# Optimization experiments

Measured on AMD Instinct MI355X. Metric: run time of the kernel, lower is better.

The kernel has to match this reference:

```python
import jax, jax.numpy as jnp
import numpy as np

B, K, N, E, D = 32, 32, 2048, 16384, 768
L_GNN, L_TR, H = 2, 4, 12
FF, VOCAB, N_ROLES, MAX_POS, N_HOPS = 3072, 25, 2, 64, 16


def setup_inputs() -> dict:
    key = jax.random.key(0)
    ks = jax.random.split(key, 32)
    s = 0.02
    inp = {
        "raw_features": jax.random.normal(ks[0], (B, K, D), jnp.float32),
        "x0": jax.random.randint(ks[1], (K, N), 0, VOCAB),
        "edge0": jax.random.randint(ks[2], (K, 2, E), 0, N),
        "batch0": jnp.sort(jax.random.randint(ks[3], (K, N), 0, B), axis=-1),
        "x1": jax.random.randint(ks[4], (K, N), 0, VOCAB),
        "edge1": jax.random.randint(ks[5], (K, 2, E), 0, N),
        "batch1": jnp.sort(jax.random.randint(ks[6], (K, N), 0, B), axis=-1),
        "role_ids": jax.random.randint(ks[7], (B, K), 0, N_ROLES),
        "position_ids": jax.random.randint(ks[8], (B, K), 0, MAX_POS),
        "hop_ids": jax.random.randint(ks[9], (B, K), 0, N_HOPS),
        # GNNForProtein params (shared across slots and both proteins)
        "amino_embed": jax.random.normal(ks[10], (VOCAB, D)) * s,
        "gnn_W": jax.random.normal(ks[11], (L_GNN, D, D)) * s,
        "gnn_b": jnp.zeros((L_GNN, D)),
        # GraphBert embeddings
        "role_emb": jax.random.normal(ks[12], (N_ROLES, D)) * s,
        "pos_emb": jax.random.normal(ks[13], (MAX_POS, D)) * s,
        "hop_emb": jax.random.normal(ks[14], (N_HOPS, D)) * s,
        "emb_ln_scale": jnp.ones((D,)),
        "emb_ln_bias": jnp.zeros((D,)),
        # GraphBert transformer layers (stacked over L_TR)
        "Wq": jax.random.normal(ks[15], (L_TR, D, D)) * s,
        "bq": jnp.zeros((L_TR, D)),
        "Wk": jax.random.normal(ks[16], (L_TR, D, D)) * s,
        "bk": jnp.zeros((L_TR, D)),
        "Wv": jax.random.normal(ks[17], (L_TR, D, D)) * s,
        "bv": jnp.zeros((L_TR, D)),
        "Wo": jax.random.normal(ks[18], (L_TR, D, D)) * s,
        "bo": jnp.zeros((L_TR, D)),
        "ln1_s": jnp.ones((L_TR, D)),
        "ln1_b": jnp.zeros((L_TR, D)),
        "W1": jax.random.normal(ks[19], (L_TR, D, FF)) * s,
        "b1": jnp.zeros((L_TR, FF)),
        "W2": jax.random.normal(ks[20], (L_TR, FF, D)) * s,
        "b2": jnp.zeros((L_TR, D)),
        "ln2_s": jnp.ones((L_TR, D)),
        "ln2_b": jnp.zeros((L_TR, D)),
    }
    return inp


def _ln(x, s, b):
    m = jnp.mean(x, -1, keepdims=True)
    v = jnp.mean(jnp.square(x - m), -1, keepdims=True)
    return (x - m) * jax.lax.rsqrt(v + 1e-12) * s + b


def _gnn(node_ids, edges, batch_idx, amino_embed, W, b):
    # One protein slot: GCN message passing + mean readout per graph in batch.
    h = amino_embed[node_ids]                      # [N, D]
    src, dst = edges[0], edges[1]
    for l in range(W.shape[0]):
        agg = jax.ops.segment_sum(h[src], dst, num_segments=N)
        h = jax.nn.relu((h + agg) @ W[l] + b[l])
    sums = jax.ops.segment_sum(h, batch_idx, num_segments=B)
    cnt = jax.ops.segment_sum(jnp.ones((h.shape[0], 1), h.dtype), batch_idx, num_segments=B)
    return sums / jnp.maximum(cnt, 1.0)           # [B, D]


def reference(raw_features, x0, edge0, batch0, x1, edge1, batch1, role_ids, position_ids, hop_ids,
              amino_embed, gnn_W, gnn_b, role_emb, pos_emb, hop_emb, emb_ln_scale, emb_ln_bias,
              Wq, bq, Wk, bk, Wv, bv, Wo, bo, ln1_s, ln1_b, W1, b1, W2, b2, ln2_s, ln2_b):
    # vmap over the K protein slots replaces the original Python loop (same math).
    gnn_v = jax.vmap(_gnn, in_axes=(0, 0, 0, None, None, None))
    p0 = gnn_v(x0, edge0, batch0, amino_embed, gnn_W, gnn_b)   # [K, B, D]
    p1 = gnn_v(x1, edge1, batch1, amino_embed, gnn_W, gnn_b)   # [K, B, D]
    feats = raw_features + jnp.transpose(p0 + p1, (1, 0, 2))   # [B, K, D]
    # GraphBert embeddings + encoder
    h = feats + role_emb[role_ids] + pos_emb[position_ids] + hop_emb[hop_ids]
    h = _ln(h, emb_ln_scale, emb_ln_bias)
    dh = D // H
    scale = float(1.0 / np.sqrt(dh))
    for l in range(Wq.shape[0]):
        q = (h @ Wq[l] + bq[l]).reshape(B, K, H, dh)
        kk = (h @ Wk[l] + bk[l]).reshape(B, K, H, dh)
        v = (h @ Wv[l] + bv[l]).reshape(B, K, H, dh)
        att = jax.nn.softmax(jnp.einsum('bqhd,bkhd->bhqk', q, kk) * scale, axis=-1)
        ctx = jnp.einsum('bhqk,bkhd->bqhd', att, v).reshape(B, K, D)
        h = _ln(h + ctx @ Wo[l] + bo[l], ln1_s[l], ln1_b[l])
        f = jax.nn.gelu(h @ W1[l] + b1[l]) @ W2[l] + b2[l]
        h = _ln(h + f, ln2_s[l], ln2_b[l])
    return h
```

## Files before the change

### kernel.cpp

```cpp
#include <hip/hip_runtime.h>
#include <hip/hip_bf16.h>
#include <math.h>

using bf16 = __hip_bfloat16;
typedef __attribute__((ext_vector_type(8))) short short8;
typedef __attribute__((ext_vector_type(4))) float floatx4;
typedef __attribute__((ext_vector_type(4))) short short4v;

#define NB   32
#define NK   32
#define NNODE 2048
#define NEDGE 16384
#define ND   768
#define NHH  12
#define DHH  64
#define NFF  3072
#define NG   64
#define LTR  4
#define VOCAB 25

static __device__ __forceinline__ float b2f(bf16 x) { return __bfloat162float(x); }
static __device__ __forceinline__ bf16 f2b(float x) { return __float2bfloat16(x); }
static __device__ __forceinline__ float bs2f(short s) {
    unsigned u = ((unsigned)(unsigned short)s) << 16;
    float f; __builtin_memcpy(&f, &u, 4); return f;
}
static __device__ __forceinline__ short f2bs(float x) {
    bf16 h = f2b(x); short s; __builtin_memcpy(&s, &h, 2); return s;
}

static __device__ __forceinline__ void load_lds16(const bf16* g, bf16* l) {
    __builtin_amdgcn_global_load_lds((const __attribute__((address_space(1))) void*)g,
                                     (__attribute__((address_space(3))) void*)l, 16, 0, 0);
}

static __device__ __forceinline__ float ldf(const void* p, size_t i, bool f32) {
    return f32 ? ((const float*)p)[i] : b2f(((const bf16*)p)[i]);
}

__global__ void detect_dtype_kernel(const void* __restrict__ eln_s, int* __restrict__ flag) {
    if (threadIdx.x == 0 && blockIdx.x == 0) {
        unsigned w = ((const unsigned*)eln_s)[0];
        flag[0] = (w == 0x3F800000u) ? 1 : 0;
    }
}

__device__ __forceinline__ void conv_tile(const void* __restrict__ src, size_t srcOff,
                                          bf16* __restrict__ dst, int R, int Cn,
                                          int tr, int tc, bool f32, int t,
                                          short (*tile)[70]) {
    int r0 = tr * 64, c0 = tc * 64;
    int rr = t >> 4, c4 = (t & 15) * 4;
    #pragma unroll
    for (int p = 0; p < 4; ++p) {
        int r = rr + p * 16;
        size_t base = srcOff + (size_t)(r0 + r) * Cn + c0 + c4;
        short4v s;
        if (f32) {
            float4 v = *(const float4*)((const float*)src + base);
            s.x = f2bs(v.x); s.y = f2bs(v.y); s.z = f2bs(v.z); s.w = f2bs(v.w);
        } else {
            s = *(const short4v*)((const short*)src + base);
        }
        tile[r][c4]     = s.x; tile[r][c4 + 1] = s.y;
        tile[r][c4 + 2] = s.z; tile[r][c4 + 3] = s.w;
    }
    __syncthreads();
    #pragma unroll
    for (int p = 0; p < 4; ++p) {
        int c = rr + p * 16;
        short4v o;
        o.x = tile[c4][c];     o.y = tile[c4 + 1][c];
        o.z = tile[c4 + 2][c]; o.w = tile[c4 + 3][c];
        *(short4v*)((short*)dst + (size_t)(c0 + c) * R + r0 + c4) = o;
    }
}

__global__ __launch_bounds__(256) void convert_gnn_kernel(const void* __restrict__ gnnW,
                                                          bf16* __restrict__ gnnT,
                                                          const int* __restrict__ flag) {
    __shared__ short tile[64][70];
    bool f32 = flag[0] != 0;
    int bid = blockIdx.x;
    int id = bid / 144, tl = bid % 144;
    conv_tile(gnnW, (size_t)id * 589824, gnnT + (size_t)id * 589824,
              768, 768, tl / 12, tl % 12, f32, threadIdx.x, tile);
}

__global__ __launch_bounds__(256) void convert_layer_kernel(
    const void* __restrict__ Wq, const void* __restrict__ Wk, const void* __restrict__ Wv,
    const void* __restrict__ Wo, const void* __restrict__ W1, const void* __restrict__ W2,
    int l, bf16* __restrict__ qkvT, bf16* __restrict__ oT,
    bf16* __restrict__ w1T, bf16* __restrict__ w2T, const int* __restrict__ flag) {
    __shared__ short tile[64][70];
    bool f32 = flag[0] != 0;
    int bid = blockIdx.x, t = threadIdx.x;
    if (bid < 432) {
        int m = bid / 144, tl = bid % 144;
        const void* src = (m == 0) ? Wq : ((m == 1) ? Wk : Wv);
        conv_tile(src, (size_t)l * 589824, qkvT + (size_t)m * 589824,
                  768, 768, tl / 12, tl % 12, f32, t, tile);
    } else if (bid < 576) {
        int tl = bid - 432;
        conv_tile(Wo, (size_t)l * 589824, oT, 768, 768, tl / 12, tl % 12, f32, t, tile);
    } else if (bid < 1152) {
        int tl = bid - 576;
        conv_tile(W1, (size_t)l * 768 * 3072, w1T, 768, 3072, tl / 48, tl % 48, f32, t, tile);
    } else {
        int tl = bid - 1152;
        conv_tile(W2, (size_t)l * 3072 * 768, w2T, 3072, 768, tl / 12, tl % 12, f32, t, tile);
    }
}

__global__ __launch_bounds__(256) void pack_bias_kernel(
    const void* __restrict__ gnnb, const void* __restrict__ bq, const void* __restrict__ bk,
    const void* __restrict__ bv, const void* __restrict__ bo, const void* __restrict__ b1,
    const void* __restrict__ b2, float* __restrict__ out, const int* __restrict__ flag) {
    bool f32 = flag[0] != 0;
    int i = blockIdx.x * 256 + threadIdx.x;
    if (i >= 1536 + LTR * 6912) return;
    float v;
    if (i < 1536) v = ldf(gnnb, i, f32);
    else {
        int j = i - 1536, l = j / 6912, r = j % 6912;
        if      (r <  768) v = ldf(bq, l * 768 + r, f32);
        else if (r < 1536) v = ldf(bk, l * 768 + r - 768, f32);
        else if (r < 2304) v = ldf(bv, l * 768 + r - 1536, f32);
        else if (r < 3072) v = ldf(bo, l * 768 + r - 2304, f32);
        else if (r < 6144) v = ldf(b1, l * 3072 + r - 3072, f32);
        else               v = ldf(b2, l * 768 + r - 6144, f32);
    }
    out[i] = v;
}

__global__ __launch_bounds__(192) void e1_kernel(const void* __restrict__ emb,
                                                 const bf16* __restrict__ w0T,
                                                 bf16* __restrict__ E1,
                                                 const int* __restrict__ flag) {
    bool f32 = flag[0] != 0;
    int v = blockIdx.x, t = threadIdx.x;
    float acc[4] = {0.f, 0.f, 0.f, 0.f};
    for (int k = 0; k < ND; k += 4) {
        float e0 = ldf(emb, (size_t)v * ND + k,     f32);
        float e1 = ldf(emb, (size_t)v * ND + k + 1, f32);
        float e2 = ldf(emb, (size_t)v * ND + k + 2, f32);
        float e3 = ldf(emb, (size_t)v * ND + k + 3, f32);
        #pragma unroll
        for (int j = 0; j < 4; ++j) {
            const short4v w = *(const short4v*)&w0T[(size_t)(t * 4 + j) * ND + k];
            acc[j] += e0 * bs2f(w.x) + e1 * bs2f(w.y) + e2 * bs2f(w.z) + e3 * bs2f(w.w);
        }
    }
    short4v o; o.x = f2bs(acc[0]); o.y = f2bs(acc[1]); o.z = f2bs(acc[2]); o.w = f2bs(acc[3]);
    ((short4v*)(E1 + (size_t)v * ND))[t] = o;
}

__global__ __launch_bounds__(256) void count_deg_kernel(const int* __restrict__ edge0,
                                                        const int* __restrict__ edge1,
                                                        int* __restrict__ deg) {
    int gid = blockIdx.x;
    int g = gid >> 6, chunk = gid & 63;
    const int* ep = (g < NK) ? (edge0 + (size_t)g * 2 * NEDGE)
                             : (edge1 + (size_t)(g - NK) * 2 * NEDGE);
    int e = chunk * 256 + threadIdx.x;
    int dst = ep[NEDGE + e];
    atomicAdd(&deg[g * NNODE + dst], 1);
}

__global__ __launch_bounds__(256) void scan_deg_kernel(int* __restrict__ deg,
                                                       int* __restrict__ indptr) {
    int g = blockIdx.x, t = threadIdx.x;
    __shared__ int sums[256];
    int loc[8]; int s = 0;
    #pragma unroll
    for (int i = 0; i < 8; ++i) { loc[i] = deg[g * NNODE + t * 8 + i]; s += loc[i]; }
    sums[t] = s; __syncthreads();
    for (int off = 1; off < 256; off <<= 1) {
        int v = (t >= off) ? sums[t - off] : 0;
        __syncthreads();
        sums[t] += v;
        __syncthreads();
    }
    int run = sums[t] - s;
    #pragma unroll
    for (int i = 0; i < 8; ++i) {
        indptr[g * (NNODE + 1) + t * 8 + i] = run;
        deg[g * NNODE + t * 8 + i] = run;
        run += loc[i];
    }
    if (t == 255) indptr[g * (NNODE + 1) + NNODE] = run;
}

__global__ __launch_bounds__(256) void fill_csr_kernel(const int* __restrict__ edge0,
                                                       const int* __restrict__ edge1,
                                                       int* __restrict__ cursor,
                                                       int* __restrict__ csr_src) {
    int gid = blockIdx.x;
    int g = gid >> 6, chunk = gid & 63;
    const int* ep = (g < NK) ? (edge0 + (size_t)g * 2 * NEDGE)
                             : (edge1 + (size_t)(g - NK) * 2 * NEDGE);
    int e = chunk * 256 + threadIdx.x;
    int src = ep[e];
    int dst = ep[NEDGE + e];
    int p = atomicAdd(&cursor[g * NNODE + dst], 1);
    csr_src[(size_t)g * NEDGE + p] = src;
}

__global__ __launch_bounds__(64) void batch_count_kernel(const int* __restrict__ batch0,
                                                         const int* __restrict__ batch1,
                                                         int* __restrict__ cnt) {
    int g = blockIdx.x;
    int b = threadIdx.x;
    if (b >= NB) return;
    const int* bp = (g < NK) ? (batch0 + (size_t)g * NNODE)
                             : (batch1 + (size_t)(g - NK) * NNODE);
    int lo = 0, hi = NNODE;
    while (lo < hi) { int mid = (lo + hi) >> 1; if (bp[mid] < b) lo = mid + 1; else hi = mid; }
    int start = lo;
    hi = NNODE;
    while (lo < hi) { int mid = (lo + hi) >> 1; if (bp[mid] < b + 1) lo = mid + 1; else hi = mid; }
    cnt[g * NB + b] = lo - start;
}

static __device__ __forceinline__ void node_block_decode(int id, int& gl, int& n) {
    int r = id & 7, q = id >> 3;
    gl = r + 8 * (q >> 11);
    n = q & 2047;
}

__global__ __launch_bounds__(192) void gnn_layer1_kernel(const int* __restrict__ x0,
                                                         const int* __restrict__ x1,
                                                         const bf16* __restrict__ E1,
                                                         const float* __restrict__ b0,
                                                         const int* __restrict__ indptr,
                                                         const int* __restrict__ csr_src,
                                                         bf16* __restrict__ hC, int g0) {
    int gl, n; node_block_decode(blockIdx.x, gl, n);
    int g = g0 + gl;
    const int* xg = (g < NK) ? (x0 + (size_t)g * NNODE) : (x1 + (size_t)(g - NK) * NNODE);
    int beg = indptr[g * (NNODE + 1) + n];
    int end = indptr[g * (NNODE + 1) + n + 1];
    const int* cs = csr_src + (size_t)g * NEDGE;
    int t = threadIdx.x;
    const short4v* E = (const short4v*)E1;
    short4v v = E[(size_t)xg[n] * 192 + t];
    float a0 = bs2f(v.x), a1 = bs2f(v.y), a2 = bs2f(v.z), a3 = bs2f(v.w);
    for (int e = beg; e < end; ++e) {
        int s = cs[e];
        short4v w = E[(size_t)xg[s] * 192 + t];
        a0 += bs2f(w.x); a1 += bs2f(w.y); a2 += bs2f(w.z); a3 += bs2f(w.w);
    }
    float4 bb = ((const float4*)b0)[t];
    short4v o;
    o.x = f2bs(fmaxf(a0 + bb.x, 0.f));
    o.y = f2bs(fmaxf(a1 + bb.y, 0.f));
    o.z = f2bs(fmaxf(a2 + bb.z, 0.f));
    o.w = f2bs(fmaxf(a3 + bb.w, 0.f));
    ((short4v*)(hC + ((size_t)gl * NNODE + n) * ND))[t] = o;
}

__global__ __launch_bounds__(192) void gnn_aggregate_kernel(const bf16* __restrict__ hC,
                                                            const int* __restrict__ indptr,
                                                            const int* __restrict__ csr_src,
                                                            bf16* __restrict__ xC, int g0) {
    int gl, n; node_block_decode(blockIdx.x, gl, n);
    int g = g0 + gl;
    int beg = indptr[g * (NNODE + 1) + n];
    int end = indptr[g * (NNODE + 1) + n + 1];
    const short4v* hg = (const short4v*)(hC + (size_t)gl * NNODE * ND);
    const int* cs = csr_src + (size_t)g * NEDGE;
    int t = threadIdx.x;
    short4v v = hg[(size_t)n * 192 + t];
    float a0 = bs2f(v.x), a1 = bs2f(v.y), a2 = bs2f(v.z), a3 = bs2f(v.w);
    for (int e = beg; e < end; ++e) {
        int s = cs[e];
        short4v w = hg[(size_t)s * 192 + t];
        a0 += bs2f(w.x); a1 += bs2f(w.y); a2 += bs2f(w.z); a3 += bs2f(w.w);
    }
    short4v o; o.x = f2bs(a0); o.y = f2bs(a1); o.z = f2bs(a2); o.w = f2bs(a3);
    ((short4v*)(xC + ((size_t)gl * NNODE + n) * ND))[t] = o;
}

__global__ __launch_bounds__(512) void gemm8_pool(const bf16* __restrict__ A,
                                                  const bf16* __restrict__ BT,
                                                  const float* __restrict__ bias,
                                                  int M, int K, int N,
                                                  const int* __restrict__ batAp,
                                                  const int* __restrict__ batBp,
                                                  float* __restrict__ pool, int g0) {
    __shared__ bf16 sA[3][256][64];
    __shared__ bf16 sB[2][128][64];
    const int nt = K >> 6;
    int nTN = N >> 7;
    int xcd = blockIdx.x & 7, jb = blockIdx.x >> 3;
    int brow = (jb / nTN) * 8 + xcd;
    int bcol = jb % nTN;
    const int row0 = brow << 8, col0 = bcol << 7;
    int t = threadIdx.x;
    int wid = t >> 6, lane = t & 63;
    int wr = wid >> 1, wc = wid & 1;
    int l15 = lane & 15, kx = lane >> 4, sw = lane & 7;

    const bf16* Abase = A + (size_t)row0 * K;
    const bf16* Bbase = BT + (size_t)col0 * K;

    auto stage = [&](const bf16* g, bf16* slot, int r0) {
        int r = r0 + (t >> 3);
        int ks = ((t & 7) ^ ((t >> 3) & 7)) << 3;
        load_lds16(g + (size_t)r * K + ks, slot + ((size_t)r0 << 6) + ((size_t)t << 3));
    };
    auto rdA = [&](int s, int i, int kh) {
        return *(const short8*)&sA[s][wr * 64 + i * 16 + l15][(((kh << 2) | kx) ^ sw) << 3];
    };
    auto rdB = [&](int s, int j, int kh) {
        return *(const short8*)&sB[s][wc * 64 + j * 16 + l15][(((kh << 2) | kx) ^ sw) << 3];
    };

    stage(Abase, &sA[0][0][0], 0);   stage(Abase, &sA[0][0][0], 64);
    stage(Abase, &sA[0][0][0], 128); stage(Abase, &sA[0][0][0], 192);
    stage(Bbase, &sB[0][0][0], 0);   stage(Bbase, &sB[0][0][0], 64);
    const bf16* gA1 = Abase + 64;
    stage(gA1, &sA[1][0][0], 0);   stage(gA1, &sA[1][0][0], 64);
    stage(gA1, &sA[1][0][0], 128); stage(gA1, &sA[1][0][0], 192);
    asm volatile("s_waitcnt vmcnt(4)" ::: "memory");
    __builtin_amdgcn_s_barrier();

    floatx4 acc[4][4] = {};
    for (int kt = 0; kt < nt; ++kt) {
        int sa = kt % 3, sb = kt & 1;
        bf16* saN = &sA[(kt + 2) % 3][0][0];
        const bf16* gA = Abase + (kt + 2) * 64;
        short8 af[4], bf[4];
        #pragma unroll
        for (int i = 0; i < 4; ++i) af[i] = rdA(sa, i, 0);
        #pragma unroll
        for (int j = 0; j < 4; ++j) bf[j] = rdB(sb, j, 0);
        if (kt + 1 < nt) {
            const bf16* gB = Bbase + (kt + 1) * 64;
            bf16* sbN = &sB[(kt + 1) & 1][0][0];
            stage(gB, sbN, 0); stage(gB, sbN, 64);
        }
        if (kt + 2 < nt) { stage(gA, saN, 0); stage(gA, saN, 64); }
        __builtin_amdgcn_s_barrier();
        asm volatile("s_waitcnt lgkmcnt(0)" ::: "memory");
        __builtin_amdgcn_s_setprio(1);
        #pragma unroll
        for (int i = 0; i < 4; ++i)
            #pragma unroll
            for (int j = 0; j < 4; ++j)
                acc[i][j] = __builtin_amdgcn_mfma_f32_16x16x32_bf16(af[i], bf[j], acc[i][j], 0, 0, 0);
        __builtin_amdgcn_s_setprio(0);
        __builtin_amdgcn_s_barrier();
        #pragma unroll
        for (int i = 0; i < 4; ++i) af[i] = rdA(sa, i, 1);
        #pragma unroll
        for (int j = 0; j < 4; ++j) bf[j] = rdB(sb, j, 1);
        if (kt + 2 < nt) { stage(gA, saN, 128); stage(gA, saN, 192); }
        __builtin_amdgcn_s_barrier();
        asm volatile("s_waitcnt lgkmcnt(0)" ::: "memory");
        __builtin_amdgcn_s_setprio(1);
        #pragma unroll
        for (int i = 0; i < 4; ++i)
            #pragma unroll
            for (int j = 0; j < 4; ++j)
                acc[i][j] = __builtin_amdgcn_mfma_f32_16x16x32_bf16(af[i], bf[j], acc[i][j], 0, 0, 0);
        __builtin_amdgcn_s_setprio(0);
        if (kt + 1 < nt) {
            if (kt + 2 < nt) asm volatile("s_waitcnt vmcnt(4)" ::: "memory");
            else             asm volatile("s_waitcnt vmcnt(0)" ::: "memory");
            __builtin_amdgcn_s_barrier();
        }
    }

    __syncthreads();
    int g = g0 + (row0 >> 11);
    const int* bp = (g < NK) ? (batAp + (size_t)g * NNODE)
                             : (batBp + (size_t)(g - NK) * NNODE);
    int nbase = row0 & (NNODE - 1);
    float* pg = pool + (size_t)g * NB * ND;
    int cb = wc * 64 + l15;
    float bv[4];
    #pragma unroll
    for (int j = 0; j < 4; ++j) bv[j] = bias[col0 + cb + j * 16];
    float* lp = (float*)sA;
    int bLo = bp[nbase], bHi = bp[nbase + 255];
    int nb = (bHi - bLo + 1) * 128;
    for (int idx = t; idx < nb; idx += 512) lp[idx] = 0.f;
    __syncthreads();
    float sums[4] = {0.f, 0.f, 0.f, 0.f};
    int curb = -1;
    #pragma unroll
    for (int i = 0; i < 4; ++i) {
        int rr = nbase + wr * 64 + i * 16 + kx * 4;
        #pragma unroll
        for (int r = 0; r < 4; ++r) {
            int b = bp[rr + r];
            if (b != curb) {
                if (curb >= 0) {
                    #pragma unroll
                    for (int j = 0; j < 4; ++j)
                        atomicAdd(&lp[(curb - bLo) * 128 + cb + j * 16], sums[j]);
                }
                curb = b;
                sums[0] = sums[1] = sums[2] = sums[3] = 0.f;
            }
            #pragma unroll
            for (int j = 0; j < 4; ++j)
                sums[j] += fmaxf(acc[i][j][r] + bv[j], 0.f);
        }
    }
    #pragma unroll
    for (int j = 0; j < 4; ++j)
        atomicAdd(&lp[(curb - bLo) * 128 + cb + j * 16], sums[j]);
    __syncthreads();
    for (int idx = t; idx < nb; idx += 512) {
        float v = lp[idx];
        if (v != 0.f)
            atomicAdd(&pg[(size_t)(bLo + (idx >> 7)) * ND + col0 + (idx & 127)], v);
    }
}

__global__ __launch_bounds__(256) void gemm_tn_sk(const bf16* __restrict__ A,
                                                  const bf16* __restrict__ BT,
                                                  const float* __restrict__ bias,
                                                  void* __restrict__ C,
                                                  int M, int K, int N, int splitK,
                                                  int act, int store) {
    __shared__ bf16 lA[2][64][32];
    __shared__ bf16 lB[2][128][32];
    int nTilesN = N >> 7, nTilesM = M >> 6;
    int tiles = nTilesM * nTilesN;
    int split = blockIdx.x / tiles;
    int jt = blockIdx.x % tiles;
    int brow = jt / nTilesN, bcol = jt % nTilesN;
    int t = threadIdx.x;
    int wave = t >> 6, lane = t & 63;
    int wr = wave >> 1, wc = wave & 1;
    int l15 = lane & 15, quad = lane >> 4;
    const int row0 = brow << 6, col0 = bcol << 7;
    const int kLen = K / splitK, kBeg = split * kLen;
    const int sr0 = t >> 2, sk0 = (t & 3) * 8;
    const bf16* Ab = A + (size_t)(row0 + sr0) * K + kBeg + sk0;
    const bf16* Bb = BT + (size_t)(col0 + sr0) * K + kBeg + sk0;
    const size_t rstride = (size_t)64 * K;

    load_lds16(Ab,           &lA[0][sr0][sk0]);
    load_lds16(Bb,           &lB[0][sr0][sk0]);
    load_lds16(Bb + rstride, &lB[0][sr0 + 64][sk0]);

    floatx4 acc[2][4] = {};
    int cur = 0;
    for (int k0 = 0; k0 < kLen; k0 += 32) {
        __syncthreads();
        if (k0 + 32 < kLen) {
            load_lds16(Ab + k0 + 32,           &lA[cur ^ 1][sr0][sk0]);
            load_lds16(Bb + k0 + 32,           &lB[cur ^ 1][sr0][sk0]);
            load_lds16(Bb + rstride + k0 + 32, &lB[cur ^ 1][sr0 + 64][sk0]);
        }
        short8 afr[2], bfr[4];
        #pragma unroll
        for (int i = 0; i < 2; ++i)
            afr[i] = *reinterpret_cast<const short8*>(&lA[cur][wr * 32 + i * 16 + l15][quad * 8]);
        #pragma unroll
        for (int j = 0; j < 4; ++j)
            bfr[j] = *reinterpret_cast<const short8*>(&lB[cur][wc * 64 + j * 16 + l15][quad * 8]);
        #pragma unroll
        for (int i = 0; i < 2; ++i)
            #pragma unroll
            for (int j = 0; j < 4; ++j)
                acc[i][j] = __builtin_amdgcn_mfma_f32_16x16x32_bf16(afr[i], bfr[j], acc[i][j], 0, 0, 0);
        cur ^= 1;
    }
    #pragma unroll
    for (int i = 0; i < 2; ++i) {
        int rbase = row0 + wr * 32 + i * 16 + quad * 4;
        #pragma unroll
        for (int j = 0; j < 4; ++j) {
            int c = col0 + wc * 64 + j * 16 + l15;
            float bv = (split == 0) ? bias[c] : 0.f;
            #pragma unroll
            for (int r = 0; r < 4; ++r) {
                float v = acc[i][j][r] + bv;
                if (act == 1) v = fmaxf(v, 0.f);
                else if (act == 2) {
                    float x = v;
                    float u = 1.5957691216057308f * (x + 0.044715f * x * x * x);
                    v = x / (1.f + __expf(-u));
                }
                size_t idx = (size_t)(rbase + r) * N + c;
                if (store == 0)      atomicAdd(&((float*)C)[idx], v);
                else if (store == 1) ((float*)C)[idx] = v;
                else                 ((bf16*)C)[idx] = f2b(v);
            }
        }
    }
}

__device__ __forceinline__ void block_ln_768(float (&x)[3], int t,
                                             const void* __restrict__ s,
                                             const void* __restrict__ b,
                                             size_t sOff, bool f32,
                                             float (&y)[3], float* red) {
    float loc = x[0] + x[1] + x[2];
    red[t] = loc; __syncthreads();
    for (int off = 128; off > 0; off >>= 1) {
        if (t < off) red[t] += red[t + off];
        __syncthreads();
    }
    float mean = red[0] * (1.f / 768.f);
    __syncthreads();
    float vs = 0.f;
    #pragma unroll
    for (int e = 0; e < 3; ++e) { float d = x[e] - mean; vs += d * d; }
    red[t] = vs; __syncthreads();
    for (int off = 128; off > 0; off >>= 1) {
        if (t < off) red[t] += red[t + off];
        __syncthreads();
    }
    float var = red[0] * (1.f / 768.f);
    __syncthreads();
    float inv = rsqrtf(var + 1e-12f);
    #pragma unroll
    for (int e = 0; e < 3; ++e) {
        int d = t + e * 256;
        y[e] = (x[e] - mean) * inv * ldf(s, sOff + d, f32) + ldf(b, sOff + d, f32);
    }
}

__global__ __launch_bounds__(256) void combine_embed_ln_kernel(
    const void* __restrict__ raw, const float* __restrict__ pooled,
    const int* __restrict__ cnt,
    const int* __restrict__ role_ids, const int* __restrict__ pos_ids, const int* __restrict__ hop_ids,
    const void* __restrict__ role_emb, const void* __restrict__ pos_emb, const void* __restrict__ hop_emb,
    const void* __restrict__ lns, const void* __restrict__ lnb,
    float* __restrict__ hT, bf16* __restrict__ hbf,
    const int* __restrict__ flag) {
    bool f32 = flag[0] != 0;
    __shared__ float red[256];
    int token = blockIdx.x;
    int b = token >> 5, k = token & 31;
    int t = threadIdx.x;
    int rid = role_ids[b * NK + k];
    int pid = pos_ids[b * NK + k];
    int hid = hop_ids[b * NK + k];
    float inv0 = 1.f / (float)max(cnt[k * NB + b], 1);
    float inv1 = 1.f / (float)max(cnt[(NK + k) * NB + b], 1);
    float x[3], y[3];
    #pragma unroll
    for (int e = 0; e < 3; ++e) {
        int d = t + e * 256;
        float p0 = pooled[((size_t)k * NB + b) * ND + d] * inv0;
        float p1 = pooled[((size_t)(NK + k) * NB + b) * ND + d] * inv1;
        x[e] = ldf(raw, (size_t)token * ND + d, f32) + p0 + p1
             + ldf(role_emb, (size_t)rid * ND + d, f32)
             + ldf(pos_emb, (size_t)pid * ND + d, f32)
             + ldf(hop_emb, (size_t)hid * ND + d, f32);
    }
    block_ln_768(x, t, lns, lnb, 0, f32, y, red);
    #pragma unroll
    for (int e = 0; e < 3; ++e) {
        int d = t + e * 256;
        hT[(size_t)token * ND + d] = y[e];
        hbf[(size_t)token * ND + d] = f2b(y[e]);
    }
}

__global__ __launch_bounds__(256) void add_ln_kernel(float* __restrict__ hT,
                                                     const void* __restrict__ lns,
                                                     const void* __restrict__ lnb,
                                                     unsigned long long sOff,
                                                     void* __restrict__ outp, int extOut,
                                                     const int* __restrict__ flag) {
    bool f32 = flag[0] != 0;
    __shared__ float red[256];
    int token = blockIdx.x;
    int t = threadIdx.x;
    float x[3], y[3];
    #pragma unroll
    for (int e = 0; e < 3; ++e) {
        int d = t + e * 256;
        x[e] = hT[(size_t)token * ND + d];
    }
    block_ln_768(x, t, lns, lnb, sOff, f32, y, red);
    #pragma unroll
    for (int e = 0; e < 3; ++e) {
        int d = t + e * 256;
        size_t idx = (size_t)token * ND + d;
        hT[idx] = y[e];
        if (extOut && f32) ((float*)outp)[idx] = y[e];
        else               ((bf16*)outp)[idx] = f2b(y[e]);
    }
}

__global__ __launch_bounds__(256) void attn_kernel(const bf16* __restrict__ qkv,
                                                   bf16* __restrict__ ctx) {
    int blk = blockIdx.x;
    int b = blk / NHH, h = blk % NHH;
    __shared__ float lq[NK][DHH], lk[NK][DHH], lv[NK][DHH];
    __shared__ float ls[NK][NK];
    int t = threadIdx.x;
    {
        int tok = t >> 3, d8 = (t & 7) * 8;
        size_t base = ((size_t)(b * NK + tok)) * (3 * ND) + h * DHH + d8;
        short8 q8 = *(const short8*)&qkv[base];
        short8 k8 = *(const short8*)&qkv[base + ND];
        short8 v8 = *(const short8*)&qkv[base + 2 * ND];
        #pragma unroll
        for (int j = 0; j < 8; ++j) {
            lq[tok][d8 + j] = bs2f(q8[j]);
            lk[tok][d8 + j] = bs2f(k8[j]);
            lv[tok][d8 + j] = bs2f(v8[j]);
        }
    }
    __syncthreads();
    const float scale = 0.125f;
    for (int i = t; i < NK * NK; i += 256) {
        int qi = i >> 5, kj = i & 31;
        float s = 0.f;
        #pragma unroll
        for (int d = 0; d < DHH; ++d) s += lq[qi][d] * lk[kj][d];
        ls[qi][kj] = s * scale;
    }
    __syncthreads();
    if (t < NK) {
        float m = -1e30f;
        for (int j = 0; j < NK; ++j) m = fmaxf(m, ls[t][j]);
        float sum = 0.f;
        for (int j = 0; j < NK; ++j) { float e = expf(ls[t][j] - m); ls[t][j] = e; sum += e; }
        float inv = 1.f / sum;
        for (int j = 0; j < NK; ++j) ls[t][j] *= inv;
    }
    __syncthreads();
    for (int i = t; i < NK * DHH; i += 256) {
        int qi = i >> 6, d = i & 63;
        float s = 0.f;
        #pragma unroll
        for (int j = 0; j < NK; ++j) s += ls[qi][j] * lv[j][d];
        ctx[((size_t)(b * NK + qi)) * ND + h * DHH + d] = f2b(s);
    }
}

extern "C" void kernel_launch(void* const* d_in, const int* in_sizes, int n_in,
                              void* d_out, int out_size, void* d_ws, size_t ws_size,
                              hipStream_t stream) {
    const void* raw      = d_in[0];
    const int*  x0       = (const int*)d_in[1];
    const int*  edge0    = (const int*)d_in[2];
    const int*  batch0   = (const int*)d_in[3];
    const int*  x1       = (const int*)d_in[4];
    const int*  edge1    = (const int*)d_in[5];
    const int*  batch1   = (const int*)d_in[6];
    const int*  role_ids = (const int*)d_in[7];
    const int*  pos_ids  = (const int*)d_in[8];
    const int*  hop_ids  = (const int*)d_in[9];
    const void* amino    = d_in[10];
    const void* gnnW     = d_in[11];
    const void* gnnb     = d_in[12];
    const void* role_emb = d_in[13];
    const void* pos_emb  = d_in[14];
    const void* hop_emb  = d_in[15];
    const void* eln_s    = d_in[16];
    const void* eln_b    = d_in[17];
    const void* Wq       = d_in[18];
    const void* bq       = d_in[19];
    const void* Wk       = d_in[20];
    const void* bk       = d_in[21];
    const void* Wv       = d_in[22];
    const void* bv       = d_in[23];
    const void* Wo       = d_in[24];
    const void* bo       = d_in[25];
    const void* ln1_s    = d_in[26];
    const void* ln1_b    = d_in[27];
    const void* W1       = d_in[28];
    const void* b1       = d_in[29];
    const void* W2       = d_in[30];
    const void* b2       = d_in[31];
    const void* ln2_s    = d_in[32];
    const void* ln2_b    = d_in[33];

    char* ws = (char*)d_ws;
    size_t off = 0;
    auto alloc = [&](size_t bytes) -> void* {
        void* p = ws + off;
        off = (off + bytes + 255) & ~(size_t)255;
        return p;
    };
    int*   dflag   = (int*)alloc(256);
    float* pooled  = (float*)alloc((size_t)NG * NB * ND * 4);
    int*   cntb    = (int*)alloc((size_t)NG * NB * 4);
    int*   indptr  = (int*)alloc((size_t)NG * (NNODE + 1) * 4);
    int*   csr_src = (int*)alloc((size_t)NG * NEDGE * 4);
    int*   degcur  = (int*)alloc((size_t)NG * NNODE * 4);
    bf16*  gnnT    = (bf16*)alloc((size_t)2 * ND * ND * 2);
    bf16*  E1      = (bf16*)alloc((size_t)VOCAB * ND * 2);
    float* biasPk  = (float*)alloc((size_t)(1536 + LTR * 6912) * 4);
    const size_t QS = (size_t)3 * ND * ND, OS = (size_t)ND * ND;
    const size_t S1 = (size_t)ND * NFF,    S2 = (size_t)NFF * ND;
    bf16*  qkvT    = (bf16*)alloc(QS * 2);
    bf16*  oT      = (bf16*)alloc(OS * 2);
    bf16*  w1T     = (bf16*)alloc(S1 * 2);
    bf16*  w2T     = (bf16*)alloc(S2 * 2);

    const size_t perG  = (size_t)NNODE * ND * 2;
    const size_t bigTR = 21 * 1024 * 1024;
    int gc = 8;
    for (int cand = 32; cand >= 8; cand >>= 1) {
        size_t bigGNN = 2 * (size_t)cand * perG;
        size_t need = off + (bigGNN > bigTR ? bigGNN : bigTR) + (1 << 20);
        if (need <= ws_size) { gc = cand; break; }
    }
    char* bigbase = (char*)alloc(2 * (size_t)gc * perG > bigTR ? 2 * (size_t)gc * perG : bigTR);
    bf16* hC = (bf16*)bigbase;
    bf16* xC = (bf16*)(bigbase + (size_t)gc * perG);
    size_t toff = 0;
    auto talloc = [&](size_t bytes) -> void* {
        void* p = bigbase + toff;
        toff = (toff + bytes + 255) & ~(size_t)255;
        return p;
    };
    float* hT    = (float*)talloc((size_t)NB * NK * ND * 4);
    bf16*  hbf   = (bf16*)talloc((size_t)NB * NK * ND * 2);
    bf16*  qkvb  = (bf16*)talloc((size_t)NB * NK * 3 * ND * 2);
    bf16*  ctxb  = (bf16*)talloc((size_t)NB * NK * ND * 2);
    bf16*  ffbuf = (bf16*)talloc((size_t)NB * NK * NFF * 2);

    auto gemm_sk = [&](const bf16* A, const bf16* BT, const float* bias, void* C,
                       int Mm, int Kk, int Nn, int splitK, int act, int store) {
        int blocks = (Mm >> 6) * (Nn >> 7) * splitK;
        gemm_tn_sk<<<blocks, 256, 0, stream>>>(A, BT, bias, C, Mm, Kk, Nn, splitK, act, store);
    };

    detect_dtype_kernel<<<1, 64, 0, stream>>>(eln_s, dflag);

    convert_gnn_kernel<<<288, 256, 0, stream>>>(gnnW, gnnT, dflag);
    pack_bias_kernel<<<(1536 + LTR * 6912 + 255) / 256, 256, 0, stream>>>(
        gnnb, bq, bk, bv, bo, b1, b2, biasPk, dflag);
    e1_kernel<<<VOCAB, 192, 0, stream>>>(amino, gnnT, E1, dflag);

    hipMemsetAsync(degcur, 0, (size_t)NG * NNODE * 4, stream);
    hipMemsetAsync(pooled, 0, (size_t)NG * NB * ND * 4, stream);
    count_deg_kernel<<<NG * 64, 256, 0, stream>>>(edge0, edge1, degcur);
    scan_deg_kernel<<<NG, 256, 0, stream>>>(degcur, indptr);
    fill_csr_kernel<<<NG * 64, 256, 0, stream>>>(edge0, edge1, degcur, csr_src);
    batch_count_kernel<<<NG, 64, 0, stream>>>(batch0, batch1, cntb);

    for (int g0 = 0; g0 < NG; g0 += gc) {
        gnn_layer1_kernel<<<gc * NNODE, 192, 0, stream>>>(x0, x1, E1, biasPk,
                                                          indptr, csr_src, hC, g0);
        gnn_aggregate_kernel<<<gc * NNODE, 192, 0, stream>>>(hC, indptr, csr_src, xC, g0);
        int blocks = ((gc * NNODE) >> 8) * (ND >> 7);
        gemm8_pool<<<blocks, 512, 0, stream>>>(xC, gnnT + (size_t)ND * ND, biasPk + ND,
                                               gc * NNODE, ND, ND,
                                               batch0, batch1, pooled, g0);
    }

    combine_embed_ln_kernel<<<NB * NK, 256, 0, stream>>>(
        raw, pooled, cntb, role_ids, pos_ids, hop_ids,
        role_emb, pos_emb, hop_emb, eln_s, eln_b, hT, hbf, dflag);

    const int M = NB * NK;
    for (int l = 0; l < LTR; ++l) {
        convert_layer_kernel<<<1728, 256, 0, stream>>>(Wq, Wk, Wv, Wo, W1, W2, l,
                                                       qkvT, oT, w1T, w2T, dflag);
        const float* lb = biasPk + 1536 + l * 6912;
        gemm_sk(hbf, qkvT, lb, qkvb, M, ND, 3 * ND, 1, 0, 2);
        attn_kernel<<<NB * NHH, 256, 0, stream>>>(qkvb, ctxb);
        gemm_sk(ctxb, oT, lb + 2304, hT, M, ND, ND, 2, 0, 0);
        add_ln_kernel<<<M, 256, 0, stream>>>(hT, ln1_s, ln1_b,
                                             (unsigned long long)l * ND, hbf, 0, dflag);
        gemm_sk(hbf, w1T, lb + 3072, ffbuf, M, ND, NFF, 1, 2, 2);
        gemm_sk(ffbuf, w2T, lb + 6144, hT, M, NFF, ND, 4, 0, 0);
        int ext = (l == LTR - 1) ? 1 : 0;
        void* outb = ext ? d_out : (void*)hbf;
        add_ln_kernel<<<M, 256, 0, stream>>>(hT, ln2_s, ln2_b,
                                             (unsigned long long)l * ND, outb, ext, dflag);
    }
}
```

Before: 1.373 ms.

## Widen GNN gather loads to 16 bytes and deepen transformer GEMM K-tile with swizzle

The GNN layer-1 and aggregate kernels now handle two nodes per 192-thread block. Each thread loads 8 bf16 values at once, and the edge loop is unrolled by two so more gathers are in flight. The split-K transformer GEMM moves from a 32-wide to a 64-wide K tile, with XOR-swizzled LDS staging to avoid bank conflicts and one barrier per tile instead of per 32-K step. This trades higher LDS usage and more registers for fewer synchronisations and wider memory transactions.

```diff
diff --git a/kernel.cpp b/kernel.cpp
--- a/kernel.cpp
+++ b/kernel.cpp
@@ -222,12 +222,6 @@
     cnt[g * NB + b] = lo - start;
 }
 
-static __device__ __forceinline__ void node_block_decode(int id, int& gl, int& n) {
-    int r = id & 7, q = id >> 3;
-    gl = r + 8 * (q >> 11);
-    n = q & 2047;
-}
-
 __global__ __launch_bounds__(192) void gnn_layer1_kernel(const int* __restrict__ x0,
                                                          const int* __restrict__ x1,
                                                          const bf16* __restrict__ E1,
@@ -235,50 +229,83 @@
                                                          const int* __restrict__ indptr,
                                                          const int* __restrict__ csr_src,
                                                          bf16* __restrict__ hC, int g0) {
-    int gl, n; node_block_decode(blockIdx.x, gl, n);
+    int id = blockIdx.x;
+    int r = id & 7, q = id >> 3;
+    int gl = r + 8 * (q >> 10);
+    int np = q & 1023;
+    int t = threadIdx.x;
+    int j = t / 96, ln = t % 96;
+    int n = np * 2 + j;
     int g = g0 + gl;
     const int* xg = (g < NK) ? (x0 + (size_t)g * NNODE) : (x1 + (size_t)(g - NK) * NNODE);
     int beg = indptr[g * (NNODE + 1) + n];
     int end = indptr[g * (NNODE + 1) + n + 1];
     const int* cs = csr_src + (size_t)g * NEDGE;
-    int t = threadIdx.x;
-    const short4v* E = (const short4v*)E1;
-    short4v v = E[(size_t)xg[n] * 192 + t];
-    float a0 = bs2f(v.x), a1 = bs2f(v.y), a2 = bs2f(v.z), a3 = bs2f(v.w);
-    for (int e = beg; e < end; ++e) {
-        int s = cs[e];
-        short4v w = E[(size_t)xg[s] * 192 + t];
-        a0 += bs2f(w.x); a1 += bs2f(w.y); a2 += bs2f(w.z); a3 += bs2f(w.w);
-    }
-    float4 bb = ((const float4*)b0)[t];
-    short4v o;
-    o.x = f2bs(fmaxf(a0 + bb.x, 0.f));
-    o.y = f2bs(fmaxf(a1 + bb.y, 0.f));
-    o.z = f2bs(fmaxf(a2 + bb.z, 0.f));
-    o.w = f2bs(fmaxf(a3 + bb.w, 0.f));
-    ((short4v*)(hC + ((size_t)gl * NNODE + n) * ND))[t] = o;
+    const short8* E = (const short8*)E1;
+    short8 v = E[(size_t)xg[n] * 96 + ln];
+    float a[8];
+    #pragma unroll
+    for (int u = 0; u < 8; ++u) a[u] = bs2f(v[u]);
+    int e = beg;
+    for (; e + 1 < end; e += 2) {
+        int s1 = cs[e], s2 = cs[e + 1];
+        short8 w1 = E[(size_t)xg[s1] * 96 + ln];
+        short8 w2 = E[(size_t)xg[s2] * 96 + ln];
+        #pragma unroll
+        for (int u = 0; u < 8; ++u) a[u] += bs2f(w1[u]) + bs2f(w2[u]);
+    }
+    if (e < end) {
+        short8 w = E[(size_t)xg[cs[e]] * 96 + ln];
+        #pragma unroll
+        for (int u = 0; u < 8; ++u) a[u] += bs2f(w[u]);
+    }
+    float4 ba = ((const float4*)b0)[ln * 2];
+    float4 bb = ((const float4*)b0)[ln * 2 + 1];
+    short8 o;
+    o[0] = f2bs(fmaxf(a[0] + ba.x, 0.f)); o[1] = f2bs(fmaxf(a[1] + ba.y, 0.f));
+    o[2] = f2bs(fmaxf(a[2] + ba.z, 0.f)); o[3] = f2bs(fmaxf(a[3] + ba.w, 0.f));
+    o[4] = f2bs(fmaxf(a[4] + bb.x, 0.f)); o[5] = f2bs(fmaxf(a[5] + bb.y, 0.f));
+    o[6] = f2bs(fmaxf(a[6] + bb.z, 0.f)); o[7] = f2bs(fmaxf(a[7] + bb.w, 0.f));
+    ((short8*)(hC + ((size_t)gl * NNODE + n) * ND))[ln] = o;
 }
 
 __global__ __launch_bounds__(192) void gnn_aggregate_kernel(const bf16* __restrict__ hC,
                                                             const int* __restrict__ indptr,
                                                             const int* __restrict__ csr_src,
                                                             bf16* __restrict__ xC, int g0) {
-    int gl, n; node_block_decode(blockIdx.x, gl, n);
+    int id = blockIdx.x;
+    int r = id & 7, q = id >> 3;
+    int gl = r + 8 * (q >> 10);
+    int np = q & 1023;
+    int t = threadIdx.x;
+    int j = t / 96, ln = t % 96;
+    int n = np * 2 + j;
     int g = g0 + gl;
     int beg = indptr[g * (NNODE + 1) + n];
     int end = indptr[g * (NNODE + 1) + n + 1];
-    const short4v* hg = (const short4v*)(hC + (size_t)gl * NNODE * ND);
+    const short8* hg = (const short8*)(hC + (size_t)gl * NNODE * ND);
     const int* cs = csr_src + (size_t)g * NEDGE;
-    int t = threadIdx.x;
-    short4v v = hg[(size_t)n * 192 + t];
-    float a0 = bs2f(v.x), a1 = bs2f(v.y), a2 = bs2f(v.z), a3 = bs2f(v.w);
-    for (int e = beg; e < end; ++e) {
-        int s = cs[e];
-        short4v w = hg[(size_t)s * 192 + t];
-        a0 += bs2f(w.x); a1 += bs2f(w.y); a2 += bs2f(w.z); a3 += bs2f(w.w);
-    }
-    short4v o; o.x = f2bs(a0); o.y = f2bs(a1); o.z = f2bs(a2); o.w = f2bs(a3);
-    ((short4v*)(xC + ((size_t)gl * NNODE + n) * ND))[t] = o;
+    short8 v = hg[(size_t)n * 96 + ln];
+    float a[8];
+    #pragma unroll
+    for (int u = 0; u < 8; ++u) a[u] = bs2f(v[u]);
+    int e = beg;
+    for (; e + 1 < end; e += 2) {
+        int s1 = cs[e], s2 = cs[e + 1];
+        short8 w1 = hg[(size_t)s1 * 96 + ln];
+        short8 w2 = hg[(size_t)s2 * 96 + ln];
+        #pragma unroll
+        for (int u = 0; u < 8; ++u) a[u] += bs2f(w1[u]) + bs2f(w2[u]);
+    }
+    if (e < end) {
+        short8 w = hg[(size_t)cs[e] * 96 + ln];
+        #pragma unroll
+        for (int u = 0; u < 8; ++u) a[u] += bs2f(w[u]);
+    }
+    short8 o;
+    #pragma unroll
+    for (int u = 0; u < 8; ++u) o[u] = f2bs(a[u]);
+    ((short8*)(xC + ((size_t)gl * NNODE + n) * ND))[ln] = o;
 }
 
 __global__ __launch_bounds__(512) void gemm8_pool(const bf16* __restrict__ A,
@@ -426,54 +453,68 @@
                                                   void* __restrict__ C,
                                                   int M, int K, int N, int splitK,
                                                   int act, int store) {
-    __shared__ bf16 lA[2][64][32];
-    __shared__ bf16 lB[2][128][32];
-    int nTilesN = N >> 7, nTilesM = M >> 6;
-    int tiles = nTilesM * nTilesN;
+    __shared__ bf16 lA[2][64][64];
+    __shared__ bf16 lB[2][128][64];
+    int nTN = N >> 7, nTM = M >> 6;
+    int tiles = nTM * nTN;
     int split = blockIdx.x / tiles;
     int jt = blockIdx.x % tiles;
-    int brow = jt / nTilesN, bcol = jt % nTilesN;
+    int brow = jt / nTN, bcol = jt % nTN;
     int t = threadIdx.x;
     int wave = t >> 6, lane = t & 63;
     int wr = wave >> 1, wc = wave & 1;
-    int l15 = lane & 15, quad = lane >> 4;
+    int l15 = lane & 15, kx = lane >> 4, sw = lane & 7;
     const int row0 = brow << 6, col0 = bcol << 7;
     const int kLen = K / splitK, kBeg = split * kLen;
-    const int sr0 = t >> 2, sk0 = (t & 3) * 8;
-    const bf16* Ab = A + (size_t)(row0 + sr0) * K + kBeg + sk0;
-    const bf16* Bb = BT + (size_t)(col0 + sr0) * K + kBeg + sk0;
-    const size_t rstride = (size_t)64 * K;
-
-    load_lds16(Ab,           &lA[0][sr0][sk0]);
-    load_lds16(Bb,           &lB[0][sr0][sk0]);
-    load_lds16(Bb + rstride, &lB[0][sr0 + 64][sk0]);
+    const int nt = kLen >> 6;
+    const bf16* Abase = A + (size_t)row0 * K + kBeg;
+    const bf16* Bbase = BT + (size_t)col0 * K + kBeg;
+
+    auto stage = [&](const bf16* gsrc, bf16* slot, int r0) {
+        int rr = r0 + (t >> 3);
+        int ks = ((t & 7) ^ (rr & 7)) << 3;
+        load_lds16(gsrc + (size_t)rr * K + ks, slot + ((size_t)r0 << 6) + ((size_t)t << 3));
+    };
+    auto stageTile = [&](int kt, int buf) {
+        const bf16* gA = Abase + kt * 64;
+        const bf16* gB = Bbase + kt * 64;
+        stage(gA, &lA[buf][0][0], 0);  stage(gA, &lA[buf][0][0], 32);
+        stage(gB, &lB[buf][0][0], 0);  stage(gB, &lB[buf][0][0], 32);
+        stage(gB, &lB[buf][0][0], 64); stage(gB, &lB[buf][0][0], 96);
+    };
+    auto rdA = [&](int s, int i, int kh) {
+        return *(const short8*)&lA[s][wr * 32 + i * 16 + l15][(((kh << 2) | kx) ^ sw) << 3];
+    };
+    auto rdB = [&](int s, int jj, int kh) {
+        return *(const short8*)&lB[s][wc * 64 + jj * 16 + l15][(((kh << 2) | kx) ^ sw) << 3];
+    };
+
+    stageTile(0, 0);
+    __syncthreads();
 
     floatx4 acc[2][4] = {};
     int cur = 0;
-    for (int k0 = 0; k0 < kLen; k0 += 32) {
+    for (int kt = 0; kt < nt; ++kt) {
+        if (kt + 1 < nt) stageTile(kt + 1, cur ^ 1);
+        #pragma unroll
+        for (int kh = 0; kh < 2; ++kh) {
+            short8 af[2], bf2[4];
+            #pragma unroll
+            for (int i = 0; i < 2; ++i) af[i] = rdA(cur, i, kh);
+            #pragma unroll
+            for (int jj = 0; jj < 4; ++jj) bf2[jj] = rdB(cur, jj, kh);
+            #pragma unroll
+            for (int i = 0; i < 2; ++i)
+                #pragma unroll
+                for (int jj = 0; jj < 4; ++jj)
+                    acc[i][jj] = __builtin_amdgcn_mfma_f32_16x16x32_bf16(af[i], bf2[jj], acc[i][jj], 0, 0, 0);
+        }
         __syncthreads();
-        if (k0 + 32 < kLen) {
-            load_lds16(Ab + k0 + 32,           &lA[cur ^ 1][sr0][sk0]);
-            load_lds16(Bb + k0 + 32,           &lB[cur ^ 1][sr0][sk0]);
-            load_lds16(Bb + rstride + k0 + 32, &lB[cur ^ 1][sr0 + 64][sk0]);
-        }
-        short8 afr[2], bfr[4];
-        #pragma unroll
-        for (int i = 0; i < 2; ++i)
-            afr[i] = *reinterpret_cast<const short8*>(&lA[cur][wr * 32 + i * 16 + l15][quad * 8]);
-        #pragma unroll
-        for (int j = 0; j < 4; ++j)
-            bfr[j] = *reinterpret_cast<const short8*>(&lB[cur][wc * 64 + j * 16 + l15][quad * 8]);
-        #pragma unroll
-        for (int i = 0; i < 2; ++i)
-            #pragma unroll
-            for (int j = 0; j < 4; ++j)
-                acc[i][j] = __builtin_amdgcn_mfma_f32_16x16x32_bf16(afr[i], bfr[j], acc[i][j], 0, 0, 0);
         cur ^= 1;
     }
     #pragma unroll
     for (int i = 0; i < 2; ++i) {
-        int rbase = row0 + wr * 32 + i * 16 + quad * 4;
+        int rbase = row0 + wr * 32 + i * 16 + kx * 4;
         #pragma unroll
         for (int j = 0; j < 4; ++j) {
             int c = col0 + wc * 64 + j * 16 + l15;
@@ -745,9 +786,9 @@
     batch_count_kernel<<<NG, 64, 0, stream>>>(batch0, batch1, cntb);
 
     for (int g0 = 0; g0 < NG; g0 += gc) {
-        gnn_layer1_kernel<<<gc * NNODE, 192, 0, stream>>>(x0, x1, E1, biasPk,
-                                                          indptr, csr_src, hC, g0);
-        gnn_aggregate_kernel<<<gc * NNODE, 192, 0, stream>>>(hC, indptr, csr_src, xC, g0);
+        gnn_layer1_kernel<<<gc * (NNODE / 2), 192, 0, stream>>>(x0, x1, E1, biasPk,
+                                                                indptr, csr_src, hC, g0);
+        gnn_aggregate_kernel<<<gc * (NNODE / 2), 192, 0, stream>>>(hC, indptr, csr_src, xC, g0);
         int blocks = ((gc * NNODE) >> 8) * (ND >> 7);
         gemm8_pool<<<blocks, 512, 0, stream>>>(xC, gnnT + (size_t)ND * ND, biasPk + ND,
                                                gc * NNODE, ND, ND,
```

After: 1.270 ms. -7.5%, faster.
